# Kernel optimization log

Measured on AMD Instinct MI355X. Metric: run time of the kernel, lower is better.

## Reference

```python
import jax, jax.numpy as jnp
import numpy as np
from jax.scipy.stats import norm

B, IN, H0, H1, OUT = 1024, 2048, 4096, 4096, 1000
EPS_CDF = 1e-5
DECAY = 0.01
NEG_SLOPE = 0.01  # LeakyReLU default slope


def setup_inputs() -> dict:
    key = jax.random.key(0)
    ks = iter(jax.random.split(key, 40))
    rn = lambda shp, s=1.0: s * jax.random.normal(next(ks), shp, dtype=jnp.float32)
    inp = {}
    inp['x'] = rn((B, IN))
    inp['z_w'] = rn((IN,), 0.02)
    for nm, (o, i) in zip(['0', '1', 'o'], [(H0, IN), (H1, H0), (OUT, H1)]):
        inp['w_mu' + nm] = rn((o, i), 0.02)
        inp['w_ls' + nm] = rn((o, i), 0.1) - 2.0  # log-sigma ~ -2 => sigma ~ 0.13
        inp['b_mu' + nm] = rn((o,), 0.02)
        inp['b_ls' + nm] = rn((o,), 0.1) - 2.0
        inp['eps_w' + nm] = rn((o, i))
        inp['eps_b' + nm] = rn((o,))
    inp['pfz0'] = jax.random.uniform(next(ks), (B, H0), dtype=jnp.float32)
    inp['pfz1'] = jax.random.uniform(next(ks), (B, H1), dtype=jnp.float32)
    inp['y'] = jax.random.randint(next(ks), (B,), 0, OUT, dtype=jnp.int32)
    inp['mz0'] = jax.random.randint(next(ks), (B, H0), 0, 2, dtype=jnp.int32)
    inp['mz1'] = jax.random.randint(next(ks), (B, H1), 0, 2, dtype=jnp.int32)
    inp['mask_mu0'] = jax.random.randint(next(ks), (H0,), 0, 2, dtype=jnp.int32)
    inp['mask_mu1'] = jax.random.randint(next(ks), (H1,), 0, 2, dtype=jnp.int32)
    inp['data_set_size'] = 60000
    return inp


def _bayes_layer(h, w_mu, w_ls, b_mu, b_ls, eps_w, eps_b, mz, mask_mu, pfz):
    sw = jnp.exp(w_ls)
    sb = jnp.exp(b_ls)
    w = w_mu + sw * eps_w          # reparameterized weight sample
    b = b_mu + sb * eps_b
    h = h @ w.T + b                # F.linear
    h = jnp.where(h >= 0, h, NEG_SLOPE * h)  # LeakyReLU
    mzf = mz.astype(h.dtype)
    m = mzf * mask_mu.astype(h.dtype)[None, :]   # [B, h]
    mult = m.shape[1] / (m.sum(1) + 1e-6)        # rescale multiplier per sample
    h = h * m * mult[:, None]
    # GFN forward-flow log-prob of the z-mask
    p = jnp.clip(pfz, 1e-6, 1.0 - 1e-6)
    flow = (mzf * jnp.log(p) + (1.0 - mzf) * jnp.log(1.0 - p)).sum()
    # Gaussian CDF likelihood of sampled weights/biases (finite-difference density)
    pw = norm.cdf(w + EPS_CDF, w_mu, sw) - norm.cdf(w - EPS_CDF, w_mu, sw)
    pb = norm.cdf(b + EPS_CDF, b_mu, sb) - norm.cdf(b - EPS_CDF, b_mu, sb)
    flow = flow + jnp.log(pw).sum() + jnp.log(pb).sum()
    return h, flow


def reference(x, z_w, w_mu0, w_ls0, b_mu0, b_ls0, eps_w0, eps_b0,
              w_mu1, w_ls1, b_mu1, b_ls1, eps_w1, eps_b1,
              w_muo, w_lso, b_muo, b_lso, eps_wo, eps_bo,
              pfz0, pfz1, y, mz0, mz1, mask_mu0, mask_mu1, data_set_size):
    loss = (x @ z_w).sum()  # total flow estimator Z
    h, f0 = _bayes_layer(x, w_mu0, w_ls0, b_mu0, b_ls0, eps_w0, eps_b0, mz0, mask_mu0, pfz0)
    loss = loss + f0
    h, f1 = _bayes_layer(h, w_mu1, w_ls1, b_mu1, b_ls1, eps_w1, eps_b1, mz1, mask_mu1, pfz1)
    loss = loss + f1
    # output BayesLinear (sampled)
    wo = w_muo + jnp.exp(w_lso) * eps_wo
    bo = b_muo + jnp.exp(b_lso) * eps_bo
    pred = h @ wo.T + bo  # [B, OUT]
    logp = jax.nn.log_softmax(pred, axis=-1)
    ce = -jnp.take_along_axis(logp, y[:, None].astype(jnp.int32), axis=1).mean()
    loss = loss + jnp.float32(data_set_size) * ce  # NLL
    wd = DECAY * ((w_mu0 ** 2).sum() + jnp.exp(w_ls0).sum()
                  + (w_mu1 ** 2).sum() + jnp.exp(w_ls1).sum())
    loss = (loss + wd) ** 2
    return pred, loss
```

## Files before the change

kernel.cpp:

```cpp
#include <hip/hip_runtime.h>
#include <math.h>

#define B_SZ 1024
#define IN_SZ 2048
#define H0_SZ 4096
#define H1_SZ 4096
#define OUT_SZ 1000

typedef _Float16 f16;
typedef __attribute__((ext_vector_type(4))) _Float16 f16x4;
typedef __attribute__((ext_vector_type(8))) _Float16 f16x8;
typedef __attribute__((ext_vector_type(4))) float f32x4;

#define OFF_N0     0ULL
#define OFF_N1     4ULL
#define OFF_MSUM0  256ULL
#define OFF_MSUM1  4352ULL
#define OFF_CPOS0  8448ULL
#define OFF_CPOS1  24832ULL
#define OFF_IDX0   41216ULL
#define OFF_IDX1   57600ULL
#define OFF_PXZ    73984ULL
#define OFF_PFL    82176ULL
#define OFF_PCE    98560ULL
#define OFF_PB     106752ULL
#define OFF_PW     107776ULL
#define OFF_BS0    370688ULL
#define OFF_BS1    387072ULL
#define OFF_BSO    403456ULL
#define OFF_XH     407552ULL
#define OFF_XL     4601856ULL
#define OFF_H0H    8796160ULL
#define OFF_H0L    17184768ULL
#define OFF_H1H    25573376ULL
#define OFF_H1L    33961984ULL
#define OFF_W0CH   42350592ULL
#define OFF_W0CL   59127808ULL
#define OFF_W1CH   75905024ULL
#define OFF_W1CL   109459456ULL
#define OFF_WOCH   143013888ULL
#define OFF_WOCL   151402496ULL
#define OFF_PART   159791104ULL

#define PSTRIDE_H  2560
#define PSTRIDE_O  1024

#define PA_W0   4096
#define PA_FL0  5120
#define PA_SX   5376
#define PA_B0   5392
#define L0_G    640
#define L0_W1   4736
#define L0_FL1  5760
#define L0_B1   5776
#define L1_G    640
#define L1_WO   1640
#define L1_BO   1644

__device__ __forceinline__ void gload_lds16(const void* g, void* l)
{
    __builtin_amdgcn_global_load_lds((const __attribute__((address_space(1))) void*)g,
                                     (__attribute__((address_space(3))) void*)l, 16, 0, 0);
}

__device__ __forceinline__ void reduce4_store(double v0, double v1, double v2, double v3,
                                              double* dst)
{
    __shared__ double sh[4][4];
    double v[4] = {v0, v1, v2, v3};
    int lane = threadIdx.x & 63, wid = threadIdx.x >> 6;
#pragma unroll
    for (int a = 0; a < 4; ++a) {
        double x = v[a];
#pragma unroll
        for (int o = 32; o > 0; o >>= 1) x += __shfl_down(x, o, 64);
        if (lane == 0) sh[a][wid] = x;
    }
    __syncthreads();
    if (threadIdx.x == 0) {
        dst[0] = sh[0][0] + sh[0][1] + sh[0][2] + sh[0][3];
        dst[1] = sh[1][0] + sh[1][1] + sh[1][2] + sh[1][3];
        dst[2] = sh[2][0] + sh[2][1] + sh[2][2] + sh[2][3];
        dst[3] = sh[3][0] + sh[3][1] + sh[3][2] + sh[3][3];
    }
}

__device__ __forceinline__ void reduce1_store(double v, double* dst)
{
    __shared__ double sh1[4];
    int lane = threadIdx.x & 63, wid = threadIdx.x >> 6;
#pragma unroll
    for (int o = 32; o > 0; o >>= 1) v += __shfl_down(v, o, 64);
    if (lane == 0) sh1[wid] = v;
    __syncthreads();
    if (threadIdx.x == 0) dst[0] = sh1[0] + sh1[1] + sh1[2] + sh1[3];
}

__global__ __launch_bounds__(1024) void idxbuild_kernel(
    const int* __restrict__ mask0, const int* __restrict__ mask1,
    int* __restrict__ cpos0, int* __restrict__ idx0, int* __restrict__ n0,
    int* __restrict__ cpos1, int* __restrict__ idx1, int* __restrict__ n1)
{
    __shared__ int sh[1024];
    const int t = threadIdx.x;
    const int pass = blockIdx.x;
    const int* mask = pass ? mask1 : mask0;
    int* cpos = pass ? cpos1 : cpos0;
    int* idx = pass ? idx1 : idx0;
    int* np = pass ? n1 : n0;
    int4 m = ((const int4*)mask)[t];
    int s = m.x + m.y + m.z + m.w;
    sh[t] = s;
    __syncthreads();
    for (int o = 1; o < 1024; o <<= 1) {
        int v = (t >= o) ? sh[t - o] : 0;
        __syncthreads();
        sh[t] += v;
        __syncthreads();
    }
    int run = sh[t] - s;
    int4 cp;
    cp.x = run; cp.y = run + m.x; cp.z = cp.y + m.y; cp.w = cp.z + m.z;
    ((int4*)cpos)[t] = cp;
    if (m.x) idx[cp.x] = 4 * t + 0;
    if (m.y) idx[cp.y] = 4 * t + 1;
    if (m.z) idx[cp.z] = 4 * t + 2;
    if (m.w) idx[cp.w] = 4 * t + 3;
    if (t == 1023) *np = sh[1023];
}


__device__ void role_splitx(int rb, const float4* x, const float4* zw,
                            f16x4* xh, f16x4* xl, double* pxz)
{
    const int n4 = B_SZ * IN_SZ / 4;
    double s = 0;
    int i = rb * 256 + threadIdx.x;
    const int stride = 256 * 256;
    for (; i < n4; i += stride) {
        float4 v = x[i];
        float4 z = zw[i & (IN_SZ / 4 - 1)];
        s += (double)((v.x * z.x + v.y * z.y) + (v.z * z.z + v.w * z.w));
        f16 h0 = (f16)v.x, h1 = (f16)v.y, h2 = (f16)v.z, h3 = (f16)v.w;
        f16x4 hv = {h0, h1, h2, h3};
        f16x4 lv = {(f16)(v.x - (float)h0), (f16)(v.y - (float)h1),
                    (f16)(v.z - (float)h2), (f16)(v.w - (float)h3)};
        xh[i] = hv; xl[i] = lv;
    }
    reduce1_store(s, pxz + rb);
}

__device__ void role_flow(int b, const int* mz, const float* pfz, const int* maskmu,
                          float* msum, double* pfl)
{
    const int4* m4 = (const int4*)(mz + (size_t)b * 4096);
    const float4* p4 = (const float4*)(pfz + (size_t)b * 4096);
    const int4* k4 = (const int4*)maskmu;
    int s = 0;
    double fl = 0;
    for (int i = threadIdx.x; i < 1024; i += 256) {
        int4 m = m4[i];
        float4 p = p4[i];
        int4 k = k4[i];
        s += m.x * k.x + m.y * k.y + m.z * k.z + m.w * k.w;
        float a0 = fminf(fmaxf(p.x, 1e-6f), 1.0f - 1e-6f);
        float a1 = fminf(fmaxf(p.y, 1e-6f), 1.0f - 1e-6f);
        float a2 = fminf(fmaxf(p.z, 1e-6f), 1.0f - 1e-6f);
        float a3 = fminf(fmaxf(p.w, 1e-6f), 1.0f - 1e-6f);
        float g0 = logf(m.x ? a0 : 1.0f - a0);
        float g1 = logf(m.y ? a1 : 1.0f - a1);
        float g2 = logf(m.z ? a2 : 1.0f - a2);
        float g3 = logf(m.w ? a3 : 1.0f - a3);
        fl += (double)((g0 + g1) + (g2 + g3));
    }
#pragma unroll
    for (int o = 32; o > 0; o >>= 1) {
        s += __shfl_down(s, o, 64);
        fl += __shfl_down(fl, o, 64);
    }
    __shared__ int shi[4];
    __shared__ double shd[4];
    if ((threadIdx.x & 63) == 0) { shi[threadIdx.x >> 6] = s; shd[threadIdx.x >> 6] = fl; }
    __syncthreads();
    if (threadIdx.x == 0) {
        msum[b] = (float)(shi[0] + shi[1] + shi[2] + shi[3]);
        pfl[b] = shd[0] + shd[1] + shd[2] + shd[3];
    }
}

template <int RED>
__device__ void role_bsample(int rb, const float* bmu, const float* bls, const float* beps,
                             float* out, int n, double* pb)
{
    int i = rb * 256 + threadIdx.x;
    float l = 0.f, e = 0.f;
    if (i < n) {
        l = bls[i]; e = beps[i];
        out[i] = fmaf(__expf(l), e, bmu[i]);
    }
    if (RED) {
        double sls = (i < n) ? (double)l : 0.0;
        double se2 = (i < n) ? (double)e * e : 0.0;
        reduce4_store(sls, se2, 0.0, 0.0, pb + (size_t)rb * 4);
    }
}

__device__ void role_w0(int r, const float* mu, const float* ls, const float* eps,
                        const int* maskR, const int* cposR, f16* hi, double* pw)
{
    const size_t rbb = (size_t)r * IN_SZ;
    const float4* m4 = (const float4*)(mu + rbb);
    const float4* l4 = (const float4*)(ls + rbb);
    const float4* e4 = (const float4*)(eps + rbb);
    const bool wr_ = maskR[r] != 0;
    const int drow = cposR[r];
    f16* hrow = hi + (size_t)drow * IN_SZ;
    double sls = 0, se2 = 0, smu2 = 0, sex = 0;
    for (int i = threadIdx.x; i < IN_SZ / 4; i += 256) {
        float4 m = m4[i], l = l4[i], e = e4[i];
        float g0 = __expf(l.x), g1 = __expf(l.y), g2 = __expf(l.z), g3 = __expf(l.w);
        float w0 = fmaf(g0, e.x, m.x), w1 = fmaf(g1, e.y, m.y);
        float w2 = fmaf(g2, e.z, m.z), w3 = fmaf(g3, e.w, m.w);
        sls += (double)((l.x + l.y) + (l.z + l.w));
        se2 += (double)((e.x * e.x + e.y * e.y) + (e.z * e.z + e.w * e.w));
        smu2 += (double)((m.x * m.x + m.y * m.y) + (m.z * m.z + m.w * m.w));
        sex += (double)((g0 + g1) + (g2 + g3));
        if (wr_) {
            f16x4 hv = {(f16)w0, (f16)w1, (f16)w2, (f16)w3};
            *(f16x4*)(hrow + i * 4) = hv;
        }
    }
    reduce4_store(sls, se2, smu2, sex, pw + (size_t)r * 4);
}

template <int ROWC, int RED>
__device__ void role_colc(int r, const float* mu, const float* ls, const float* eps,
                          const int* maskR, const int* cposR,
                          const int* maskC, const int* cposC, const int* pNc,
                          f16* hi, double* pw, f16* ldsH)
{
    const size_t rbb = (size_t)r * 4096;
    const float4* m4 = (const float4*)(mu + rbb);
    const float4* l4 = (const float4*)(ls + rbb);
    const float4* e4 = (const float4*)(eps + rbb);
    const bool wr_ = ROWC ? (maskR[r] != 0) : true;
    const int drow = ROWC ? cposR[r] : r;
    const int t = threadIdx.x;
    const f16x8 z8 = {0, 0, 0, 0, 0, 0, 0, 0};
    for (int i = t; i < 512; i += 256) ((f16x8*)ldsH)[i] = z8;
    __syncthreads();
    double sls = 0, se2 = 0, smu2 = 0, sex = 0;
    for (int i = t; i < 1024; i += 256) {
        float4 m = m4[i], l = l4[i], e = e4[i];
        float g0 = __expf(l.x), g1 = __expf(l.y), g2 = __expf(l.z), g3 = __expf(l.w);
        float w0 = fmaf(g0, e.x, m.x), w1 = fmaf(g1, e.y, m.y);
        float w2 = fmaf(g2, e.z, m.z), w3 = fmaf(g3, e.w, m.w);
        if (RED) {
            sls += (double)((l.x + l.y) + (l.z + l.w));
            se2 += (double)((e.x * e.x + e.y * e.y) + (e.z * e.z + e.w * e.w));
            smu2 += (double)((m.x * m.x + m.y * m.y) + (m.z * m.z + m.w * m.w));
            sex += (double)((g0 + g1) + (g2 + g3));
        }
        if (wr_) {
            int4 mc = ((const int4*)maskC)[i];
            int4 cp = ((const int4*)cposC)[i];
            if (mc.x) ldsH[cp.x] = (f16)w0;
            if (mc.y) ldsH[cp.y] = (f16)w1;
            if (mc.z) ldsH[cp.z] = (f16)w2;
            if (mc.w) ldsH[cp.w] = (f16)w3;
        }
    }
    __syncthreads();
    if (wr_) {
        const int n8 = ((*pNc + 127) >> 7) << 4;
        f16x8* hd = (f16x8*)(hi + (size_t)drow * 4096);
        for (int i = t; i < n8; i += 256) hd[i] = ((const f16x8*)ldsH)[i];
    }
    if (RED) reduce4_store(sls, se2, smu2, sex, pw + (size_t)r * 4);
}

template <int NSPLIT>
__device__ void gemm_body(int bid, f16* ldsbase,
                          const f16* Ah, const f16* Al, int SA,
                          const f16* Wh, int SW,
                          const int* pN, int NFIX, const int* pK, int KFIX,
                          float* P0, float* P1, float* P2, float* P3,
                          float* P4, float* P5, float* P6, float* P7, int pstride)
{
    const int c8 = bid & 7, j = bid >> 3;
    int nt, mt, z;
    if (NSPLIT == 4) {
        const int p = c8 + 8 * (j % 10);
        nt = p >> 2; z = p & 3; mt = j / 10;
    } else {
        const int p = c8 + 8 * (j & 7);
        nt = p >> 3; z = p & 7; mt = j >> 3;
    }
    const int nvalid = pN ? *pN : NFIX;
    const int bn = nt * 128;
    if (bn >= nvalid) return;
    const int bm = mt * 128;
    const int kvalid = pK ? *pK : KFIX;
    const int ktiles = (kvalid + 31) >> 5;
    const int prt = (ktiles + NSPLIT - 1) / NSPLIT;
    const int kt0 = z * prt;
    const int kt1 = min(ktiles, kt0 + prt);
    float* Cf = (z == 0) ? P0 : (z == 1) ? P1 : (z == 2) ? P2 : (z == 3) ? P3
              : (z == 4) ? P4 : (z == 5) ? P5 : (z == 6) ? P6 : P7;

    const int tid = threadIdx.x;
    const int wv = tid >> 6, lane = tid & 63;
    const int wr = wv >> 1, wc = wv & 1;
    const int l15 = lane & 15, l4 = lane >> 4;

    const f16* sg[6];
    int ldst[6];
#pragma unroll
    for (int i = 0; i < 6; ++i) {
        const int c = wv * 6 + i;
        const int plane = c >> 3, cidx = c & 7;
        const f16* base = (plane == 0) ? Ah : (plane == 1) ? Al : Wh;
        const int S_ = (plane < 2) ? SA : SW;
        const int rowb = (plane < 2) ? bm : bn;
        sg[i] = base + (size_t)(rowb + cidx * 16 + l15) * S_ + l4 * 8;
        ldst[i] = c * 512 + lane * 8;
    }

#define STAGE(KT, B) do { \
        _Pragma("unroll") \
        for (int i_ = 0; i_ < 6; ++i_) \
            gload_lds16(sg[i_] + (size_t)(KT) * 32, ldsbase + (B) * 12288 + ldst[i_]); \
    } while (0)

    f32x4 acc[4][4];
#pragma unroll
    for (int m = 0; m < 4; ++m)
#pragma unroll
        for (int n = 0; n < 4; ++n) acc[m][n] = (f32x4){0.f, 0.f, 0.f, 0.f};

    if (kt0 < kt1) {
        STAGE(kt0, 0);
        int cur = 0;
        for (int kt = kt0; kt < kt1; ++kt) {
            asm volatile("s_waitcnt vmcnt(0)" ::: "memory");
            __builtin_amdgcn_s_barrier();
            __builtin_amdgcn_sched_barrier(0);
            if (kt + 1 < kt1) STAGE(kt + 1, cur ^ 1);
            __builtin_amdgcn_sched_barrier(0);
            const f16* L = ldsbase + cur * 12288;
            f16x8 ah[4], al[4], wh[4];
#pragma unroll
            for (int m = 0; m < 4; ++m) {
                ah[m] = *(const f16x8*)(L + (wr * 4 + m) * 512 + lane * 8);
                al[m] = *(const f16x8*)(L + 4096 + (wr * 4 + m) * 512 + lane * 8);
            }
#pragma unroll
            for (int n = 0; n < 4; ++n)
                wh[n] = *(const f16x8*)(L + 8192 + (wc * 4 + n) * 512 + lane * 8);
#pragma unroll
            for (int m = 0; m < 4; ++m)
#pragma unroll
                for (int n = 0; n < 4; ++n)
                    acc[m][n] = __builtin_amdgcn_mfma_f32_16x16x32_f16(ah[m], wh[n], acc[m][n], 0, 0, 0);
#pragma unroll
            for (int m = 0; m < 4; ++m)
#pragma unroll
                for (int n = 0; n < 4; ++n)
                    acc[m][n] = __builtin_amdgcn_mfma_f32_16x16x32_f16(al[m], wh[n], acc[m][n], 0, 0, 0);
            cur ^= 1;
        }
    }
#undef STAGE

#pragma unroll
    for (int n = 0; n < 4; ++n) {
        const int c = bn + wc * 64 + n * 16 + l15;
        if (c >= pstride) continue;
#pragma unroll
        for (int m = 0; m < 4; ++m)
#pragma unroll
            for (int j2 = 0; j2 < 4; ++j2) {
                const int row = bm + wr * 64 + m * 16 + l4 * 4 + j2;
                Cf[(size_t)row * pstride + c] = acc[m][n][j2];
            }
    }
}

__global__ __launch_bounds__(256) void prepA_kernel(
    const float* __restrict__ x, const float* __restrict__ zw,
    const float* __restrict__ wmu0, const float* __restrict__ wls0, const float* __restrict__ weps0,
    const float* __restrict__ bmu0, const float* __restrict__ bls0, const float* __restrict__ beps0,
    const float* __restrict__ pfz0, const int* __restrict__ mz0,
    const int* __restrict__ mmu0, const int* __restrict__ cpos0,
    f16* __restrict__ xh, f16* __restrict__ xl, f16* __restrict__ w0ch,
    float* __restrict__ bs0, float* __restrict__ msum0,
    double* __restrict__ PXZ, double* __restrict__ PFL,
    double* __restrict__ PB, double* __restrict__ PW)
{
    const int b = blockIdx.x;
    if (b < PA_W0) {
        role_w0(b, wmu0, wls0, weps0, mmu0, cpos0, w0ch, PW);
    } else if (b < PA_FL0) {
        role_flow(b - PA_W0, mz0, pfz0, mmu0, msum0, PFL);
    } else if (b < PA_SX) {
        role_splitx(b - PA_FL0, (const float4*)x, (const float4*)zw,
                    (f16x4*)xh, (f16x4*)xl, PXZ);
    } else {
        role_bsample<1>(b - PA_SX, bmu0, bls0, beps0, bs0, H0_SZ, PB);
    }
}

__global__ __launch_bounds__(256, 3) void gemmL0_kernel(
    const f16* __restrict__ xh, const f16* __restrict__ xl, const f16* __restrict__ w0ch,
    const int* __restrict__ n0p,
    float* __restrict__ A0, float* __restrict__ A1,
    float* __restrict__ A2, float* __restrict__ A3,
    const float* __restrict__ wmu1, const float* __restrict__ wls1, const float* __restrict__ weps1,
    const float* __restrict__ bmu1, const float* __restrict__ bls1, const float* __restrict__ beps1,
    const float* __restrict__ pfz1, const int* __restrict__ mz1,
    const int* __restrict__ mmu0, const int* __restrict__ mmu1,
    const int* __restrict__ cpos0, const int* __restrict__ cpos1,
    f16* __restrict__ w1ch, float* __restrict__ bs1, float* __restrict__ msum1,
    double* __restrict__ PFL, double* __restrict__ PB, double* __restrict__ PW)
{
    __shared__ __align__(16) f16 lds[2][12288];
    const int b = blockIdx.x;
    if (b < L0_G) {
        gemm_body<4>(b, &lds[0][0], xh, xl, IN_SZ, w0ch, IN_SZ, n0p, 0, nullptr, IN_SZ,
                     A0, A1, A2, A3, nullptr, nullptr, nullptr, nullptr, PSTRIDE_H);
    } else if (b < L0_W1) {
        role_colc<1, 1>(b - L0_G, wmu1, wls1, weps1, mmu1, cpos1, mmu0, cpos0, n0p,
                        w1ch, PW + (size_t)4096 * 4, &lds[0][0]);
    } else if (b < L0_FL1) {
        role_flow(b - L0_W1, mz1, pfz1, mmu1, msum1, PFL + 1024);
    } else {
        role_bsample<1>(b - L0_FL1, bmu1, bls1, beps1, bs1, H1_SZ, PB + 16 * 4);
    }
}

__global__ __launch_bounds__(256, 3) void gemmL1_kernel(
    const f16* __restrict__ h0h, const f16* __restrict__ h0l, const f16* __restrict__ w1ch,
    const int* __restrict__ n1p, const int* __restrict__ n0p,
    float* __restrict__ B0, float* __restrict__ B1,
    float* __restrict__ B2, float* __restrict__ B3,
    const float* __restrict__ wmuo, const float* __restrict__ wlso, const float* __restrict__ wepso,
    const float* __restrict__ bmuo, const float* __restrict__ blso, const float* __restrict__ bepso,
    const int* __restrict__ mmu1, const int* __restrict__ cpos1,
    f16* __restrict__ woch, float* __restrict__ bso)
{
    __shared__ __align__(16) f16 lds[2][12288];
    const int b = blockIdx.x;
    if (b < L1_G) {
        gemm_body<4>(b, &lds[0][0], h0h, h0l, 4096, w1ch, 4096, n1p, 0, n0p, 0,
                     B0, B1, B2, B3, nullptr, nullptr, nullptr, nullptr, PSTRIDE_H);
    } else if (b < L1_WO) {
        role_colc<0, 0>(b - L1_G, wmuo, wlso, wepso, nullptr, nullptr, mmu1, cpos1, n1p,
                        woch, nullptr, &lds[0][0]);
    } else {
        role_bsample<0>(b - L1_WO, bmuo, blso, bepso, bso, OUT_SZ, nullptr);
    }
}

__global__ __launch_bounds__(256, 3) void gemmLo_kernel(
    const f16* __restrict__ h1h, const f16* __restrict__ h1l, const f16* __restrict__ woch,
    const int* __restrict__ n1p,
    float* __restrict__ Q0, float* __restrict__ Q1, float* __restrict__ Q2, float* __restrict__ Q3,
    float* __restrict__ Q4, float* __restrict__ Q5, float* __restrict__ Q6, float* __restrict__ Q7)
{
    __shared__ __align__(16) f16 lds[2][12288];
    gemm_body<8>(blockIdx.x, &lds[0][0], h1h, h1l, 4096, woch, 4096, nullptr, OUT_SZ, n1p, 0,
                 Q0, Q1, Q2, Q3, Q4, Q5, Q6, Q7, PSTRIDE_O);
}

__global__ __launch_bounds__(256) void combine4_kernel(
    const float* __restrict__ PA, const float* __restrict__ PB,
    const float* __restrict__ PC, const float* __restrict__ PD, int pstride,
    const float* __restrict__ bsamp, const int* __restrict__ idx,
    const int* __restrict__ mz, const float* __restrict__ msum,
    const int* __restrict__ pN,
    f16* __restrict__ Chh, f16* __restrict__ Chl)
{
    const int nv = *pN;
    const int bn = blockIdx.x * 64;
    const int bm = blockIdx.y * 64;
    const int t = threadIdx.x;
    const int c0 = bn + (t & 15) * 4;
    const int r0 = bm + (t >> 4);
#pragma unroll
    for (int rr = 0; rr < 4; ++rr) {
        const int row = r0 + rr * 16;
        const float mult = 4096.0f / (msum[row] + 1e-6f);
        float sv[4] = {0.f, 0.f, 0.f, 0.f};
        if (c0 < pstride) {
            float4 a = *(const float4*)(PA + (size_t)row * pstride + c0);
            float4 b = *(const float4*)(PB + (size_t)row * pstride + c0);
            float4 c = *(const float4*)(PC + (size_t)row * pstride + c0);
            float4 d = *(const float4*)(PD + (size_t)row * pstride + c0);
            sv[0] = (a.x + b.x) + (c.x + d.x);
            sv[1] = (a.y + b.y) + (c.y + d.y);
            sv[2] = (a.z + b.z) + (c.z + d.z);
            sv[3] = (a.w + b.w) + (c.w + d.w);
        }
        f16 hh[4], ll[4];
#pragma unroll
        for (int jj = 0; jj < 4; ++jj) {
            const int c = c0 + jj;
            float v = 0.f;
            if (c < nv) {
                const int orig = idx[c];
                v = sv[jj] + bsamp[orig];
                v = v >= 0.f ? v : 0.01f * v;
                v = v * (float)mz[(size_t)row * 4096 + orig] * mult;
            }
            hh[jj] = (f16)v;
            ll[jj] = (f16)(v - (float)hh[jj]);
        }
        f16x4 hv = {hh[0], hh[1], hh[2], hh[3]};
        f16x4 lv = {ll[0], ll[1], ll[2], ll[3]};
        *(f16x4*)(Chh + (size_t)row * 4096 + c0) = hv;
        *(f16x4*)(Chl + (size_t)row * 4096 + c0) = lv;
    }
}

__global__ __launch_bounds__(256) void ce_fused8_kernel(
    const float* __restrict__ Q0, const float* __restrict__ Q1,
    const float* __restrict__ Q2, const float* __restrict__ Q3,
    const float* __restrict__ Q4, const float* __restrict__ Q5,
    const float* __restrict__ Q6, const float* __restrict__ Q7,
    const float* __restrict__ bso, const int* __restrict__ y,
    float* __restrict__ pred, double* __restrict__ pce)
{
    const int b = blockIdx.x;
    float mx = -1e30f;
    for (int jj = threadIdx.x; jj < OUT_SZ; jj += 256) {
        const size_t o = (size_t)b * PSTRIDE_O + jj;
        float v = ((Q0[o] + Q1[o]) + (Q2[o] + Q3[o]))
                + ((Q4[o] + Q5[o]) + (Q6[o] + Q7[o])) + bso[jj];
        pred[(size_t)b * OUT_SZ + jj] = v;
        mx = fmaxf(mx, v);
    }
#pragma unroll
    for (int o = 32; o > 0; o >>= 1) mx = fmaxf(mx, __shfl_down(mx, o, 64));
    __shared__ float sm[4];
    if ((threadIdx.x & 63) == 0) sm[threadIdx.x >> 6] = mx;
    __syncthreads();
    mx = fmaxf(fmaxf(sm[0], sm[1]), fmaxf(sm[2], sm[3]));
    double se = 0;
    for (int jj = threadIdx.x; jj < OUT_SZ; jj += 256)
        se += (double)__expf(pred[(size_t)b * OUT_SZ + jj] - mx);
#pragma unroll
    for (int o = 32; o > 0; o >>= 1) se += __shfl_down(se, o, 64);
    __shared__ double sd[4];
    if ((threadIdx.x & 63) == 0) sd[threadIdx.x >> 6] = se;
    __syncthreads();
    if (threadIdx.x == 0) {
        double lse = (double)mx + log(sd[0] + sd[1] + sd[2] + sd[3]);
        pce[b] = lse - (double)pred[(size_t)b * OUT_SZ + y[b]];
    }
}

__global__ __launch_bounds__(256) void finalize_kernel(
    const double* __restrict__ PXZ, const double* __restrict__ PFL,
    const double* __restrict__ PCE, const double* __restrict__ PB,
    const double* __restrict__ PW, const int* __restrict__ dss, float* __restrict__ out)
{
    const int t = threadIdx.x;
    double xz = 0, fl = 0, ce = 0, ls = 0, e2 = 0, mu2 = 0, ex = 0;
    xz += PXZ[t];
    for (int i = t; i < 2048; i += 256) fl += PFL[i];
    for (int i = t; i < 1024; i += 256) ce += PCE[i];
    for (int i = t; i < 8192; i += 256) {
        const double* p = PW + (size_t)i * 4;
        ls += p[0]; e2 += p[1]; mu2 += p[2]; ex += p[3];
    }
    if (t < 32) { ls += PB[t * 4]; e2 += PB[t * 4 + 1]; }
    __shared__ double sh[7][4];
    double v[7] = {xz, fl, ce, ls, e2, mu2, ex};
    const int lane = t & 63, wid = t >> 6;
#pragma unroll
    for (int a = 0; a < 7; ++a) {
        double x = v[a];
#pragma unroll
        for (int o = 32; o > 0; o >>= 1) x += __shfl_down(x, o, 64);
        if (lane == 0) sh[a][wid] = x;
    }
    __syncthreads();
    if (t == 0) {
        double T[7];
#pragma unroll
        for (int a = 0; a < 7; ++a) T[a] = sh[a][0] + sh[a][1] + sh[a][2] + sh[a][3];
        const double NTOT = 25174016.0;
        double cst = NTOT * (log(2.0e-5) - 0.91893853320467274178);
        double loss = T[0]
                    + cst - T[3] - 0.5 * T[4]
                    + T[1]
                    + (double)(*dss) * (T[2] / (double)B_SZ)
                    + 0.01 * (T[5] + T[6]);
        out[(size_t)B_SZ * OUT_SZ] = (float)(loss * loss);
    }
}

extern "C" void kernel_launch(void* const* d_in, const int* in_sizes, int n_in,
                              void* d_out, int out_size, void* d_ws, size_t ws_size,
                              hipStream_t stream)
{
    const float* x = (const float*)d_in[0];
    const float* zw = (const float*)d_in[1];
    const float* wmu0 = (const float*)d_in[2];
    const float* wls0 = (const float*)d_in[3];
    const float* bmu0 = (const float*)d_in[4];
    const float* bls0 = (const float*)d_in[5];
    const float* weps0 = (const float*)d_in[6];
    const float* beps0 = (const float*)d_in[7];
    const float* wmu1 = (const float*)d_in[8];
    const float* wls1 = (const float*)d_in[9];
    const float* bmu1 = (const float*)d_in[10];
    const float* bls1 = (const float*)d_in[11];
    const float* weps1 = (const float*)d_in[12];
    const float* beps1 = (const float*)d_in[13];
    const float* wmuo = (const float*)d_in[14];
    const float* wlso = (const float*)d_in[15];
    const float* bmuo = (const float*)d_in[16];
    const float* blso = (const float*)d_in[17];
    const float* wepso = (const float*)d_in[18];
    const float* bepso = (const float*)d_in[19];
    const float* pfz0 = (const float*)d_in[20];
    const float* pfz1 = (const float*)d_in[21];
    const int* y = (const int*)d_in[22];
    const int* mz0 = (const int*)d_in[23];
    const int* mz1 = (const int*)d_in[24];
    const int* mmu0 = (const int*)d_in[25];
    const int* mmu1 = (const int*)d_in[26];
    const int* dss = (const int*)d_in[27];

    char* ws = (char*)d_ws;
    int* n0p = (int*)(ws + OFF_N0);
    int* n1p = (int*)(ws + OFF_N1);
    float* msum0 = (float*)(ws + OFF_MSUM0);
    float* msum1 = (float*)(ws + OFF_MSUM1);
    int* cpos0 = (int*)(ws + OFF_CPOS0);
    int* cpos1 = (int*)(ws + OFF_CPOS1);
    int* idx0 = (int*)(ws + OFF_IDX0);
    int* idx1 = (int*)(ws + OFF_IDX1);
    double* PXZ = (double*)(ws + OFF_PXZ);
    double* PFL = (double*)(ws + OFF_PFL);
    double* PCE = (double*)(ws + OFF_PCE);
    double* PB = (double*)(ws + OFF_PB);
    double* PW = (double*)(ws + OFF_PW);
    float* bs0 = (float*)(ws + OFF_BS0);
    float* bs1 = (float*)(ws + OFF_BS1);
    float* bso = (float*)(ws + OFF_BSO);
    f16* xh = (f16*)(ws + OFF_XH);
    f16* xl = (f16*)(ws + OFF_XL);
    f16* h0h = (f16*)(ws + OFF_H0H);
    f16* h0l = (f16*)(ws + OFF_H0L);
    f16* h1h = (f16*)(ws + OFF_H1H);
    f16* h1l = (f16*)(ws + OFF_H1L);
    f16* w0ch = (f16*)(ws + OFF_W0CH);
    f16* w1ch = (f16*)(ws + OFF_W1CH);
    f16* woch = (f16*)(ws + OFF_WOCH);
    float* out = (float*)d_out;

    float* A0 = (float*)(ws + OFF_H1H);
    float* A1 = (float*)(ws + OFF_PART);
    float* A2 = (float*)(ws + OFF_W0CL);
    float* A3 = (float*)(ws + OFF_W1CL);
    float* B0 = (float*)(ws + OFF_W0CH);
    float* B1 = (float*)(ws + OFF_W0CL);
    float* B2 = (float*)(ws + OFF_W1CL);
    float* B3 = (float*)(ws + OFF_PART);
    float* Q[8];
    for (int i = 0; i < 8; ++i) Q[i] = (float*)(ws + OFF_W0CH + (size_t)i * 4194304ULL);

    idxbuild_kernel<<<2, 1024, 0, stream>>>(mmu0, mmu1, cpos0, idx0, n0p, cpos1, idx1, n1p);

    prepA_kernel<<<PA_B0, 256, 0, stream>>>(
        x, zw, wmu0, wls0, weps0, bmu0, bls0, beps0,
        pfz0, mz0, mmu0, cpos0,
        xh, xl, w0ch, bs0, msum0, PXZ, PFL, PB, PW);

    gemmL0_kernel<<<L0_B1, 256, 0, stream>>>(
        xh, xl, w0ch, n0p, A0, A1, A2, A3,
        wmu1, wls1, weps1, bmu1, bls1, beps1,
        pfz1, mz1, mmu0, mmu1, cpos0, cpos1,
        w1ch, bs1, msum1, PFL, PB, PW);
    combine4_kernel<<<dim3(64, 16), 256, 0, stream>>>(
        A0, A1, A2, A3, PSTRIDE_H, bs0, idx0, mz0, msum0, n0p, h0h, h0l);

    gemmL1_kernel<<<L1_BO, 256, 0, stream>>>(
        h0h, h0l, w1ch, n1p, n0p, B0, B1, B2, B3,
        wmuo, wlso, wepso, bmuo, blso, bepso,
        mmu1, cpos1, woch, bso);
    combine4_kernel<<<dim3(64, 16), 256, 0, stream>>>(
        B0, B1, B2, B3, PSTRIDE_H, bs1, idx1, mz1, msum1, n1p, h1h, h1l);

    gemmLo_kernel<<<512, 256, 0, stream>>>(
        h1h, h1l, woch, n1p, Q[0], Q[1], Q[2], Q[3], Q[4], Q[5], Q[6], Q[7]);

    ce_fused8_kernel<<<B_SZ, 256, 0, stream>>>(Q[0], Q[1], Q[2], Q[3], Q[4], Q[5], Q[6], Q[7],
                                               bso, y, out, PCE);
    finalize_kernel<<<1, 256, 0, stream>>>(PXZ, PFL, PCE, PB, PW, dss, out);
}
```

Before: 256.0 us.

## Fuse bias/LeakyReLU/mask epilogue into hidden GEMMs, drop split-K and combine kernels

The two hidden-layer GEMMs no longer split K four ways into fp32 partial buffers. Each tile now computes the full K range and applies bias, LeakyReLU, mask rescaling and the hi/lo f16 split directly in its epilogue, so both combine4 launches go away. The hidden GEMMs also drop LDS double buffering for a single stage so more blocks fit per CU (launch bounds raised to 5). This removes partial-sum write/read traffic and two launches, but cuts GEMM block count from 640 to 160 with longer serial K loops and no load/compute overlap. That can leave the GPU underfilled or latency-bound, and the epilogue now writes scalar f16 stores instead of vectorised ones.

```diff
diff --git a/kernel.cpp b/kernel.cpp
--- a/kernel.cpp
+++ b/kernel.cpp
@@ -35,27 +35,23 @@
 #define OFF_H1H    25573376ULL
 #define OFF_H1L    33961984ULL
 #define OFF_W0CH   42350592ULL
-#define OFF_W0CL   59127808ULL
 #define OFF_W1CH   75905024ULL
-#define OFF_W1CL   109459456ULL
 #define OFF_WOCH   143013888ULL
-#define OFF_WOCL   151402496ULL
 #define OFF_PART   159791104ULL
 
-#define PSTRIDE_H  2560
 #define PSTRIDE_O  1024
 
 #define PA_W0   4096
 #define PA_FL0  5120
 #define PA_SX   5376
 #define PA_B0   5392
-#define L0_G    640
-#define L0_W1   4736
-#define L0_FL1  5760
-#define L0_B1   5776
-#define L1_G    640
-#define L1_WO   1640
-#define L1_BO   1644
+#define F0_G    160
+#define F0_W1   4256
+#define F0_FL1  5280
+#define F0_B1   5296
+#define F1_G    160
+#define F1_WO   1160
+#define F1_BO   1164
 
 __device__ __forceinline__ void gload_lds16(const void* g, void* l)
 {
@@ -279,20 +275,23 @@
     if (RED) reduce4_store(sls, se2, smu2, sex, pw + (size_t)r * 4);
 }
 
-template <int NSPLIT>
+template <int NSPLIT, int EPI, int DBUF>
 __device__ void gemm_body(int bid, f16* ldsbase,
                           const f16* Ah, const f16* Al, int SA,
                           const f16* Wh, int SW,
-                          const int* pN, int NFIX, const int* pK, int KFIX,
+                          const int* pN, int NFIX,
+                          const int* pK, int KFIX,
                           float* P0, float* P1, float* P2, float* P3,
-                          float* P4, float* P5, float* P6, float* P7, int pstride)
-{
-    const int c8 = bid & 7, j = bid >> 3;
+                          float* P4, float* P5, float* P6, float* P7, int pstride,
+                          const float* bsamp, const int* idx,
+                          const int* mz, const float* msum,
+                          f16* Chh, f16* Chl, int SC)
+{
     int nt, mt, z;
-    if (NSPLIT == 4) {
-        const int p = c8 + 8 * (j % 10);
-        nt = p >> 2; z = p & 3; mt = j / 10;
+    if (NSPLIT == 1) {
+        nt = bid % 20; mt = bid / 20; z = 0;
     } else {
+        const int c8 = bid & 7, j = bid >> 3;
         const int p = c8 + 8 * (j & 7);
         nt = p >> 3; z = p & 7; mt = j >> 3;
     }
@@ -338,51 +337,96 @@
 #pragma unroll
         for (int n = 0; n < 4; ++n) acc[m][n] = (f32x4){0.f, 0.f, 0.f, 0.f};
 
+#define COMPUTE(L) do { \
+        f16x8 ah[4], al[4], wh[4]; \
+        _Pragma("unroll") \
+        for (int m = 0; m < 4; ++m) { \
+            ah[m] = *(const f16x8*)((L) + (wr * 4 + m) * 512 + lane * 8); \
+            al[m] = *(const f16x8*)((L) + 4096 + (wr * 4 + m) * 512 + lane * 8); \
+        } \
+        _Pragma("unroll") \
+        for (int n = 0; n < 4; ++n) \
+            wh[n] = *(const f16x8*)((L) + 8192 + (wc * 4 + n) * 512 + lane * 8); \
+        _Pragma("unroll") \
+        for (int m = 0; m < 4; ++m) \
+            _Pragma("unroll") \
+            for (int n = 0; n < 4; ++n) \
+                acc[m][n] = __builtin_amdgcn_mfma_f32_16x16x32_f16(ah[m], wh[n], acc[m][n], 0, 0, 0); \
+        _Pragma("unroll") \
+        for (int m = 0; m < 4; ++m) \
+            _Pragma("unroll") \
+            for (int n = 0; n < 4; ++n) \
+                acc[m][n] = __builtin_amdgcn_mfma_f32_16x16x32_f16(al[m], wh[n], acc[m][n], 0, 0, 0); \
+    } while (0)
+
     if (kt0 < kt1) {
-        STAGE(kt0, 0);
-        int cur = 0;
-        for (int kt = kt0; kt < kt1; ++kt) {
-            asm volatile("s_waitcnt vmcnt(0)" ::: "memory");
-            __builtin_amdgcn_s_barrier();
-            __builtin_amdgcn_sched_barrier(0);
-            if (kt + 1 < kt1) STAGE(kt + 1, cur ^ 1);
-            __builtin_amdgcn_sched_barrier(0);
-            const f16* L = ldsbase + cur * 12288;
-            f16x8 ah[4], al[4], wh[4];
+        if (DBUF) {
+            STAGE(kt0, 0);
+            int cur = 0;
+            for (int kt = kt0; kt < kt1; ++kt) {
+                asm volatile("s_waitcnt vmcnt(0)" ::: "memory");
+                __builtin_amdgcn_s_barrier();
+                __builtin_amdgcn_sched_barrier(0);
+                if (kt + 1 < kt1) STAGE(kt + 1, cur ^ 1);
+                __builtin_amdgcn_sched_barrier(0);
+                const f16* L = ldsbase + cur * 12288;
+                COMPUTE(L);
+                cur ^= 1;
+            }
+        } else {
+            for (int kt = kt0; kt < kt1; ++kt) {
+                STAGE(kt, 0);
+                asm volatile("s_waitcnt vmcnt(0)" ::: "memory");
+                __builtin_amdgcn_s_barrier();
+                __builtin_amdgcn_sched_barrier(0);
+                const f16* L = ldsbase;
+                COMPUTE(L);
+                __builtin_amdgcn_sched_barrier(0);
+                __builtin_amdgcn_s_barrier();
+            }
+        }
+    }
+#undef STAGE
+#undef COMPUTE
+
+    if (EPI == 0) {
+#pragma unroll
+        for (int n = 0; n < 4; ++n) {
+            const int c = bn + wc * 64 + n * 16 + l15;
+            const bool cv = c < nvalid;
+            const int orig = cv ? idx[c] : 0;
+            const float bias = cv ? bsamp[orig] : 0.f;
 #pragma unroll
             for (int m = 0; m < 4; ++m) {
-                ah[m] = *(const f16x8*)(L + (wr * 4 + m) * 512 + lane * 8);
-                al[m] = *(const f16x8*)(L + 4096 + (wr * 4 + m) * 512 + lane * 8);
+#pragma unroll
+                for (int j2 = 0; j2 < 4; ++j2) {
+                    const int row = bm + wr * 64 + m * 16 + l4 * 4 + j2;
+                    float v = 0.f;
+                    if (cv) {
+                        v = acc[m][n][j2] + bias;
+                        v = v >= 0.f ? v : 0.01f * v;
+                        const float mult = 4096.0f / (msum[row] + 1e-6f);
+                        v = v * (float)mz[(size_t)row * 4096 + orig] * mult;
+                    }
+                    const f16 hh = (f16)v;
+                    Chh[(size_t)row * SC + c] = hh;
+                    Chl[(size_t)row * SC + c] = (f16)(v - (float)hh);
+                }
             }
-#pragma unroll
-            for (int n = 0; n < 4; ++n)
-                wh[n] = *(const f16x8*)(L + 8192 + (wc * 4 + n) * 512 + lane * 8);
+        }
+    } else {
+#pragma unroll
+        for (int n = 0; n < 4; ++n) {
+            const int c = bn + wc * 64 + n * 16 + l15;
+            if (c >= pstride) continue;
 #pragma unroll
             for (int m = 0; m < 4; ++m)
 #pragma unroll
-                for (int n = 0; n < 4; ++n)
-                    acc[m][n] = __builtin_amdgcn_mfma_f32_16x16x32_f16(ah[m], wh[n], acc[m][n], 0, 0, 0);
-#pragma unroll
-            for (int m = 0; m < 4; ++m)
-#pragma unroll
-                for (int n = 0; n < 4; ++n)
-                    acc[m][n] = __builtin_amdgcn_mfma_f32_16x16x32_f16(al[m], wh[n], acc[m][n], 0, 0, 0);
-            cur ^= 1;
+                for (int j2 = 0; j2 < 4; ++j2) {
+                    const int row = bm + wr * 64 + m * 16 + l4 * 4 + j2;
+                    Cf[(size_t)row * pstride + c] = acc[m][n][j2];
+                }
         }
-    }
-#undef STAGE
-
-#pragma unroll
-    for (int n = 0; n < 4; ++n) {
-        const int c = bn + wc * 64 + n * 16 + l15;
-        if (c >= pstride) continue;
-#pragma unroll
-        for (int m = 0; m < 4; ++m)
-#pragma unroll
-            for (int j2 = 0; j2 < 4; ++j2) {
-                const int row = bm + wr * 64 + m * 16 + l4 * 4 + j2;
-                Cf[(size_t)row * pstride + c] = acc[m][n][j2];
-            }
     }
 }
 
@@ -410,11 +454,12 @@
     }
 }
 
-__global__ __launch_bounds__(256, 3) void gemmL0_kernel(
+__global__ __launch_bounds__(256, 5) void gemmL0_kernel(
     const f16* __restrict__ xh, const f16* __restrict__ xl, const f16* __restrict__ w0ch,
     const int* __restrict__ n0p,
-    float* __restrict__ A0, float* __restrict__ A1,
-    float* __restrict__ A2, float* __restrict__ A3,
+    const float* __restrict__ bs0, const int* __restrict__ idx0,
+    const int* __restrict__ mz0, const float* __restrict__ msum0,
+    f16* __restrict__ h0h, f16* __restrict__ h0l,
     const float* __restrict__ wmu1, const float* __restrict__ wls1, const float* __restrict__ weps1,
     const float* __restrict__ bmu1, const float* __restrict__ bls1, const float* __restrict__ beps1,
     const float* __restrict__ pfz1, const int* __restrict__ mz1,
@@ -423,41 +468,44 @@
     f16* __restrict__ w1ch, float* __restrict__ bs1, float* __restrict__ msum1,
     double* __restrict__ PFL, double* __restrict__ PB, double* __restrict__ PW)
 {
-    __shared__ __align__(16) f16 lds[2][12288];
+    __shared__ __align__(16) f16 lds[12288];
     const int b = blockIdx.x;
-    if (b < L0_G) {
-        gemm_body<4>(b, &lds[0][0], xh, xl, IN_SZ, w0ch, IN_SZ, n0p, 0, nullptr, IN_SZ,
-                     A0, A1, A2, A3, nullptr, nullptr, nullptr, nullptr, PSTRIDE_H);
-    } else if (b < L0_W1) {
-        role_colc<1, 1>(b - L0_G, wmu1, wls1, weps1, mmu1, cpos1, mmu0, cpos0, n0p,
-                        w1ch, PW + (size_t)4096 * 4, &lds[0][0]);
-    } else if (b < L0_FL1) {
-        role_flow(b - L0_W1, mz1, pfz1, mmu1, msum1, PFL + 1024);
+    if (b < F0_G) {
+        gemm_body<1, 0, 0>(b, &lds[0], xh, xl, IN_SZ, w0ch, IN_SZ, n0p, 0, nullptr, IN_SZ,
+                           nullptr, nullptr, nullptr, nullptr, nullptr, nullptr, nullptr, nullptr, 0,
+                           bs0, idx0, mz0, msum0, h0h, h0l, 4096);
+    } else if (b < F0_W1) {
+        role_colc<1, 1>(b - F0_G, wmu1, wls1, weps1, mmu1, cpos1, mmu0, cpos0, n0p,
+                        w1ch, PW + (size_t)4096 * 4, &lds[0]);
+    } else if (b < F0_FL1) {
+        role_flow(b - F0_W1, mz1, pfz1, mmu1, msum1, PFL + 1024);
     } else {
-        role_bsample<1>(b - L0_FL1, bmu1, bls1, beps1, bs1, H1_SZ, PB + 16 * 4);
-    }
-}
-
-__global__ __launch_bounds__(256, 3) void gemmL1_kernel(
+        role_bsample<1>(b - F0_FL1, bmu1, bls1, beps1, bs1, H1_SZ, PB + 16 * 4);
+    }
+}
+
+__global__ __launch_bounds__(256, 5) void gemmL1_kernel(
     const f16* __restrict__ h0h, const f16* __restrict__ h0l, const f16* __restrict__ w1ch,
     const int* __restrict__ n1p, const int* __restrict__ n0p,
-    float* __restrict__ B0, float* __restrict__ B1,
-    float* __restrict__ B2, float* __restrict__ B3,
+    const float* __restrict__ bs1, const int* __restrict__ idx1,
+    const int* __restrict__ mz1, const float* __restrict__ msum1,
+    f16* __restrict__ h1h, f16* __restrict__ h1l,
     const float* __restrict__ wmuo, const float* __restrict__ wlso, const float* __restrict__ wepso,
     const float* __restrict__ bmuo, const float* __restrict__ blso, const float* __restrict__ bepso,
     const int* __restrict__ mmu1, const int* __restrict__ cpos1,
     f16* __restrict__ woch, float* __restrict__ bso)
 {
-    __shared__ __align__(16) f16 lds[2][12288];
+    __shared__ __align__(16) f16 lds[12288];
     const int b = blockIdx.x;
-    if (b < L1_G) {
-        gemm_body<4>(b, &lds[0][0], h0h, h0l, 4096, w1ch, 4096, n1p, 0, n0p, 0,
-                     B0, B1, B2, B3, nullptr, nullptr, nullptr, nullptr, PSTRIDE_H);
-    } else if (b < L1_WO) {
-        role_colc<0, 0>(b - L1_G, wmuo, wlso, wepso, nullptr, nullptr, mmu1, cpos1, n1p,
-                        woch, nullptr, &lds[0][0]);
+    if (b < F1_G) {
+        gemm_body<1, 0, 0>(b, &lds[0], h0h, h0l, 4096, w1ch, 4096, n1p, 0, n0p, 0,
+                           nullptr, nullptr, nullptr, nullptr, nullptr, nullptr, nullptr, nullptr, 0,
+                           bs1, idx1, mz1, msum1, h1h, h1l, 4096);
+    } else if (b < F1_WO) {
+        role_colc<0, 0>(b - F1_G, wmuo, wlso, wepso, nullptr, nullptr, mmu1, cpos1, n1p,
+                        woch, nullptr, &lds[0]);
     } else {
-        role_bsample<0>(b - L1_WO, bmuo, blso, bepso, bso, OUT_SZ, nullptr);
+        role_bsample<0>(b - F1_WO, bmuo, blso, bepso, bso, OUT_SZ, nullptr);
     }
 }
 
@@ -468,58 +516,9 @@
     float* __restrict__ Q4, float* __restrict__ Q5, float* __restrict__ Q6, float* __restrict__ Q7)
 {
     __shared__ __align__(16) f16 lds[2][12288];
-    gemm_body<8>(blockIdx.x, &lds[0][0], h1h, h1l, 4096, woch, 4096, nullptr, OUT_SZ, n1p, 0,
-                 Q0, Q1, Q2, Q3, Q4, Q5, Q6, Q7, PSTRIDE_O);
-}
-
-__global__ __launch_bounds__(256) void combine4_kernel(
-    const float* __restrict__ PA, const float* __restrict__ PB,
-    const float* __restrict__ PC, const float* __restrict__ PD, int pstride,
-    const float* __restrict__ bsamp, const int* __restrict__ idx,
-    const int* __restrict__ mz, const float* __restrict__ msum,
-    const int* __restrict__ pN,
-    f16* __restrict__ Chh, f16* __restrict__ Chl)
-{
-    const int nv = *pN;
-    const int bn = blockIdx.x * 64;
-    const int bm = blockIdx.y * 64;
-    const int t = threadIdx.x;
-    const int c0 = bn + (t & 15) * 4;
-    const int r0 = bm + (t >> 4);
-#pragma unroll
-    for (int rr = 0; rr < 4; ++rr) {
-        const int row = r0 + rr * 16;
-        const float mult = 4096.0f / (msum[row] + 1e-6f);
-        float sv[4] = {0.f, 0.f, 0.f, 0.f};
-        if (c0 < pstride) {
-            float4 a = *(const float4*)(PA + (size_t)row * pstride + c0);
-            float4 b = *(const float4*)(PB + (size_t)row * pstride + c0);
-            float4 c = *(const float4*)(PC + (size_t)row * pstride + c0);
-            float4 d = *(const float4*)(PD + (size_t)row * pstride + c0);
-            sv[0] = (a.x + b.x) + (c.x + d.x);
-            sv[1] = (a.y + b.y) + (c.y + d.y);
-            sv[2] = (a.z + b.z) + (c.z + d.z);
-            sv[3] = (a.w + b.w) + (c.w + d.w);
-        }
-        f16 hh[4], ll[4];
-#pragma unroll
-        for (int jj = 0; jj < 4; ++jj) {
-            const int c = c0 + jj;
-            float v = 0.f;
-            if (c < nv) {
-                const int orig = idx[c];
-                v = sv[jj] + bsamp[orig];
-                v = v >= 0.f ? v : 0.01f * v;
-                v = v * (float)mz[(size_t)row * 4096 + orig] * mult;
-            }
-            hh[jj] = (f16)v;
-            ll[jj] = (f16)(v - (float)hh[jj]);
-        }
-        f16x4 hv = {hh[0], hh[1], hh[2], hh[3]};
-        f16x4 lv = {ll[0], ll[1], ll[2], ll[3]};
-        *(f16x4*)(Chh + (size_t)row * 4096 + c0) = hv;
-        *(f16x4*)(Chl + (size_t)row * 4096 + c0) = lv;
-    }
+    gemm_body<8, 1, 1>(blockIdx.x, &lds[0][0], h1h, h1l, 4096, woch, 4096, nullptr, OUT_SZ, n1p, 0,
+                       Q0, Q1, Q2, Q3, Q4, Q5, Q6, Q7, PSTRIDE_O,
+                       nullptr, nullptr, nullptr, nullptr, nullptr, nullptr, 0);
 }
 
 __global__ __launch_bounds__(256) void ce_fused8_kernel(
@@ -661,14 +660,6 @@
     f16* woch = (f16*)(ws + OFF_WOCH);
     float* out = (float*)d_out;
 
-    float* A0 = (float*)(ws + OFF_H1H);
-    float* A1 = (float*)(ws + OFF_PART);
-    float* A2 = (float*)(ws + OFF_W0CL);
-    float* A3 = (float*)(ws + OFF_W1CL);
-    float* B0 = (float*)(ws + OFF_W0CH);
-    float* B1 = (float*)(ws + OFF_W0CL);
-    float* B2 = (float*)(ws + OFF_W1CL);
-    float* B3 = (float*)(ws + OFF_PART);
     float* Q[8];
     for (int i = 0; i < 8; ++i) Q[i] = (float*)(ws + OFF_W0CH + (size_t)i * 4194304ULL);
 
@@ -679,20 +670,16 @@
         pfz0, mz0, mmu0, cpos0,
         xh, xl, w0ch, bs0, msum0, PXZ, PFL, PB, PW);
 
-    gemmL0_kernel<<<L0_B1, 256, 0, stream>>>(
-        xh, xl, w0ch, n0p, A0, A1, A2, A3,
+    gemmL0_kernel<<<F0_B1, 256, 0, stream>>>(
+        xh, xl, w0ch, n0p, bs0, idx0, mz0, msum0, h0h, h0l,
         wmu1, wls1, weps1, bmu1, bls1, beps1,
         pfz1, mz1, mmu0, mmu1, cpos0, cpos1,
         w1ch, bs1, msum1, PFL, PB, PW);
-    combine4_kernel<<<dim3(64, 16), 256, 0, stream>>>(
-        A0, A1, A2, A3, PSTRIDE_H, bs0, idx0, mz0, msum0, n0p, h0h, h0l);
-
-    gemmL1_kernel<<<L1_BO, 256, 0, stream>>>(
-        h0h, h0l, w1ch, n1p, n0p, B0, B1, B2, B3,
+
+    gemmL1_kernel<<<F1_BO, 256, 0, stream>>>(
+        h0h, h0l, w1ch, n1p, n0p, bs1, idx1, mz1, msum1, h1h, h1l,
         wmuo, wlso, wepso, bmuo, blso, bepso,
         mmu1, cpos1, woch, bso);
-    combine4_kernel<<<dim3(64, 16), 256, 0, stream>>>(
-        B0, B1, B2, B3, PSTRIDE_H, bs1, idx1, mz1, msum1, n1p, h1h, h1l);
 
     gemmLo_kernel<<<512, 256, 0, stream>>>(
         h1h, h1l, woch, n1p, Q[0], Q[1], Q[2], Q[3], Q[4], Q[5], Q[6], Q[7]);
```

After: 695.9 us. 172% more time.
